# Kernel tuning notes

Measured on AMD Instinct MI355X. Metric: run time of the kernel, lower is better.

## Reference

```python
import jax, jax.numpy as jnp
import numpy as np

B, S, D = 2, 2048, 2048
H, HKV = 16, 4
GROUPS = H // HKV
RQ, RKV = 1024, 512
DH, DR = 192, 64          # q_head_dim, rope dim
DN = DH - DR              # nrope dim = 128
DV = 128                  # v head dim
EPS = 1e-20


def setup_inputs() -> dict:
    key = jax.random.key(0)
    ks = jax.random.split(key, 8)
    inp = {
        "hidden_states": jax.random.normal(ks[0], (B, S, D), jnp.float32),
        # causal mask (0 = masked), as used by masked_fill(mask == 0, -inf)
        "attention_mask": jnp.tril(jnp.ones((S, S), jnp.int32))[None, None],
        "w_qa": jax.random.normal(ks[1], (D, RQ), jnp.float32) * 0.02,
        "b_qa": jnp.zeros((RQ,), jnp.float32),
        "g_q": jnp.ones((RQ,), jnp.float32),
        "w_qb": jax.random.normal(ks[2], (RQ, H * DH), jnp.float32) * 0.02,
        "b_qb": jnp.zeros((H * DH,), jnp.float32),
        "w_kva": jax.random.normal(ks[3], (D, RKV + DR), jnp.float32) * 0.02,
        "b_kva": jnp.zeros((RKV + DR,), jnp.float32),
        "g_kv": jnp.ones((RKV,), jnp.float32),
        "w_kvb": jax.random.normal(ks[4], (RKV, HKV * (DN + DV)), jnp.float32) * 0.02,
        "b_kvb": jnp.zeros((HKV * (DN + DV),), jnp.float32),
        "w_o": jax.random.normal(ks[5], (H * DV, D), jnp.float32) * 0.02,
        "b_o": jnp.zeros((D,), jnp.float32),
    }
    return inp


def _rmsnorm(x, g, eps=EPS):
    var = jnp.mean(x * x, axis=-1, keepdims=True)
    return x * jax.lax.rsqrt(var + eps) * g


def _rope_cos_sin(seq_len, dim, base=10000.0, dtype=jnp.float32):
    inv_freq = 1.0 / (base ** (jnp.arange(0, dim, 2, dtype=jnp.float32) / dim))
    t = jnp.arange(seq_len, dtype=jnp.float32)
    freqs = jnp.outer(t, inv_freq)                    # [S, dim/2]
    emb = jnp.concatenate([freqs, freqs], axis=-1)    # [S, dim]
    return jnp.cos(emb).astype(dtype), jnp.sin(emb).astype(dtype)


def _apply_rope(x, cos, sin):
    # x: [..., S, dr]; rotate_half convention
    d2 = x.shape[-1] // 2
    x1, x2 = x[..., :d2], x[..., d2:]
    rot = jnp.concatenate([-x2, x1], axis=-1)
    return x * cos + rot * sin


def reference(hidden_states, attention_mask, w_qa, b_qa, g_q, w_qb, b_qb,
              w_kva, b_kva, g_kv, w_kvb, b_kvb, w_o, b_o):
    b, s, _ = hidden_states.shape
    # --- Q: LoRA down -> RMSNorm -> LoRA up ---
    q_a = hidden_states @ w_qa + b_qa                         # [B,S,RQ]
    q_b = _rmsnorm(q_a, g_q) @ w_qb + b_qb                    # [B,S,H*DH]
    q_b = q_b.reshape(b, s, H, DH).transpose(0, 2, 1, 3)      # [B,H,S,DH]
    q_nrope, q_rope = q_b[..., :DN], q_b[..., DN:]
    # --- KV: LoRA down, split latent / shared rope key ---
    kv_a = hidden_states @ w_kva + b_kva                      # [B,S,RKV+DR]
    kv_c, k_rope = kv_a[..., :RKV], kv_a[..., RKV:]
    kv_b = _rmsnorm(kv_c, g_kv) @ w_kvb + b_kvb               # [B,S,HKV*(DN+DV)]
    kv_b = kv_b.reshape(b, s, HKV, DN + DV).transpose(0, 2, 1, 3)
    k_nrope, value_states = kv_b[..., :DN], kv_b[..., DN:]    # [B,HKV,S,DN/DV]
    # --- split RoPE ---
    cos, sin = _rope_cos_sin(s, DR, dtype=hidden_states.dtype)
    q_rope = _apply_rope(q_rope, cos, sin)                    # [B,H,S,DR]
    k_rope = _apply_rope(k_rope[:, None], cos, sin)           # [B,1,S,DR]
    # --- assemble heads (rope part first, matching source concat order) ---
    query_states = jnp.concatenate([q_rope, q_nrope], axis=-1)            # [B,H,S,DH]
    key_states = jnp.concatenate(
        [jnp.broadcast_to(k_rope, (b, HKV, s, DR)), k_nrope], axis=-1)    # [B,HKV,S,DH]
    # --- GQA expand kv heads ---
    key_states = jnp.repeat(key_states, GROUPS, axis=1)                   # [B,H,S,DH]
    value_states = jnp.repeat(value_states, GROUPS, axis=1)               # [B,H,S,DV]
    # --- attention ---
    scores = jnp.einsum('bhqd,bhkd->bhqk', query_states, key_states)
    scores = scores / jnp.sqrt(jnp.asarray(DH, scores.dtype))
    scores = jnp.where(attention_mask == 0, jnp.asarray(-1e9, scores.dtype), scores)
    weights = jax.nn.softmax(scores, axis=-1)
    attn_out = jnp.einsum('bhqk,bhkd->bhqd', weights, value_states)       # [B,H,S,DV]
    attn_out = attn_out.transpose(0, 2, 1, 3).reshape(b, s, H * DV)
    return attn_out @ w_o + b_o
```

## Files before the change

### kernel.cpp

```cpp
#include <hip/hip_runtime.h>
#include <hip/hip_bf16.h>
#include <stdint.h>

#define DEV static __device__ __forceinline__

typedef __attribute__((ext_vector_type(8))) short bf16x8;
typedef __attribute__((ext_vector_type(4))) float f32x4;
typedef __attribute__((ext_vector_type(16))) float f32x16;

constexpr int Bc = 2, Sc = 2048, Dc = 2048;
constexpr int Hc = 16, HKVc = 4;
constexpr int RQc = 1024, RKVc = 512;
constexpr int DHc = 192, DRc = 64, DVc = 128;

DEV unsigned short f2bf(float f) {
  union { float f; uint32_t u; } v; v.f = f;
  uint32_t r = v.u + 0x7FFFu + ((v.u >> 16) & 1u);
  return (unsigned short)(r >> 16);
}
DEV float bf2f(unsigned short u) {
  union { uint32_t u; float f; } v; v.u = ((uint32_t)u) << 16;
  return v.f;
}

DEV void gload_lds16(const unsigned short* g, unsigned short* l) {
  __builtin_amdgcn_global_load_lds(
      (const __attribute__((address_space(1))) unsigned int*)g,
      (__attribute__((address_space(3))) unsigned int*)l, 16, 0, 0);
}

__global__ void f2b_kernel(const float* __restrict__ in, unsigned short* __restrict__ out, int n) {
  int stride = gridDim.x * blockDim.x;
  for (int i = blockIdx.x * blockDim.x + threadIdx.x; i * 4 < n; i += stride) {
    float4 v = reinterpret_cast<const float4*>(in)[i];
    union { unsigned short u[4]; uint64_t q; } pk;
    pk.u[0] = f2bf(v.x); pk.u[1] = f2bf(v.y); pk.u[2] = f2bf(v.z); pk.u[3] = f2bf(v.w);
    reinterpret_cast<uint64_t*>(out)[i] = pk.q;
  }
}

__global__ void wtrans_kernel(const float* __restrict__ in, unsigned short* __restrict__ out,
                              int R, int C) {
  __shared__ float tile[32][33];
  const int c0 = blockIdx.x * 32, r0 = blockIdx.y * 32;
  const int tx = threadIdx.x & 31, ty = threadIdx.x >> 5;
#pragma unroll
  for (int i = 0; i < 32; i += 8)
    tile[ty + i][tx] = in[(size_t)(r0 + ty + i) * C + c0 + tx];
  __syncthreads();
#pragma unroll
  for (int i = 0; i < 32; i += 8)
    out[(size_t)(c0 + ty + i) * R + r0 + tx] = f2bf(tile[tx][ty + i]);
}

__global__ void rope_table_kernel(float* __restrict__ cosT, float* __restrict__ sinT) {
  int idx = blockIdx.x * blockDim.x + threadIdx.x;
  if (idx >= Sc * DRc) return;
  int t = idx >> 6;
  int j = idx & 63;
  float inv = exp2f(-13.287712379549449f * (float)(j & 31) * (1.0f / 32.0f));
  float f = (float)t * inv;
  cosT[idx] = cosf(f);
  sinT[idx] = sinf(f);
}

template<int R>
__global__ void rmsnorm_kernel(const float* __restrict__ in, int istride,
                               const float* __restrict__ g, unsigned short* __restrict__ out) {
  int row = blockIdx.x;
  const float* x = in + (size_t)row * istride;
  float ss = 0.f;
  for (int j = threadIdx.x; j < R; j += 256) { float v = x[j]; ss += v * v; }
  for (int off = 32; off; off >>= 1) ss += __shfl_down(ss, off, 64);
  __shared__ float wsum[4];
  if ((threadIdx.x & 63) == 0) wsum[threadIdx.x >> 6] = ss;
  __syncthreads();
  float tot = wsum[0] + wsum[1] + wsum[2] + wsum[3];
  float rs = rsqrtf(tot * (1.0f / R) + 1e-20f);
  for (int j = threadIdx.x; j < R; j += 256)
    out[(size_t)row * R + j] = f2bf(x[j] * rs * g[j]);
}

template<bool OUT_BF16, bool NG>
__global__ __launch_bounds__(256)
void gemm_tn_kernel(const unsigned short* __restrict__ A, const unsigned short* __restrict__ Bt,
                    const float* __restrict__ bias, void* __restrict__ Cout,
                    int M, int N, int K) {
  __shared__ __align__(16) unsigned short As[2][128 * 64];
  __shared__ __align__(16) unsigned short Bs[2][128 * 64];
  const int t = threadIdx.x, lane = t & 63, wave = t >> 6;
  const int wm = wave >> 1, wn = wave & 1;
  const int m0 = blockIdx.x * 128, n0 = blockIdx.y * 128;
  const int fr = lane & 15, fo = (lane >> 4) * 8, rg = lane >> 4;
  const int srow = lane >> 3;
  const int scol = (lane & 7) * 8;

  const unsigned short* Ap[4];
  const unsigned short* Bp[4];
#pragma unroll
  for (int i = 0; i < 4; ++i) {
    const int ar = m0 + wave * 32 + i * 8 + srow;
    Ap[i] = A + (size_t)ar * K + scol;
    int br = n0 + wave * 32 + i * 8 + srow;
    if (NG) br = br < N ? br : N - 1;
    Bp[i] = Bt + (size_t)br * K + scol;
  }

  auto stage = [&](int buf, int k0) {
#pragma unroll
    for (int i = 0; i < 4; ++i) {
      gload_lds16(Ap[i] + k0, &As[buf][(wave * 32 + i * 8) * 64]);
      gload_lds16(Bp[i] + k0, &Bs[buf][(wave * 32 + i * 8) * 64]);
    }
  };

  f32x4 acc[4][4] = {};
  const int nt = K >> 6;

  stage(0, 0);
  for (int tt = 0; tt < nt; ++tt) {
    const int cur = tt & 1;
    if (tt + 1 < nt) {
      stage(cur ^ 1, (tt + 1) * 64);
      asm volatile("s_waitcnt vmcnt(8)" ::: "memory");
    } else {
      asm volatile("s_waitcnt vmcnt(0)" ::: "memory");
    }
    __syncthreads();
#pragma unroll
    for (int kk = 0; kk < 64; kk += 32) {
      bf16x8 af[4], bf[4];
#pragma unroll
      for (int m = 0; m < 4; ++m)
        af[m] = *reinterpret_cast<const bf16x8*>(&As[cur][(wm * 64 + m * 16 + fr) * 64 + kk + fo]);
#pragma unroll
      for (int n = 0; n < 4; ++n)
        bf[n] = *reinterpret_cast<const bf16x8*>(&Bs[cur][(wn * 64 + n * 16 + fr) * 64 + kk + fo]);
      __builtin_amdgcn_s_setprio(1);
#pragma unroll
      for (int m = 0; m < 4; ++m)
#pragma unroll
        for (int n = 0; n < 4; ++n)
          acc[m][n] = __builtin_amdgcn_mfma_f32_16x16x32_bf16(af[m], bf[n], acc[m][n], 0, 0, 0);
      __builtin_amdgcn_s_setprio(0);
    }
    __syncthreads();
  }

#pragma unroll
  for (int m = 0; m < 4; ++m) {
    const int row = m0 + wm * 64 + m * 16 + rg * 4;
#pragma unroll
    for (int n = 0; n < 4; ++n) {
      const int col = n0 + wn * 64 + n * 16 + fr;
      if (NG && col >= N) continue;
      const float bb = bias[col];
#pragma unroll
      for (int r = 0; r < 4; ++r) {
        float v = acc[m][n][r] + bb;
        if (OUT_BF16)
          reinterpret_cast<unsigned short*>(Cout)[(size_t)(row + r) * N + col] = f2bf(v);
        else
          reinterpret_cast<float*>(Cout)[(size_t)(row + r) * N + col] = v;
      }
    }
  }
}

__global__ __launch_bounds__(256)
void gemm_qfuse_kernel(const unsigned short* __restrict__ A, const unsigned short* __restrict__ Bt,
                       const float* __restrict__ bias,
                       const float* __restrict__ cosT, const float* __restrict__ sinT,
                       unsigned short* __restrict__ Qt, int M, int N, int K) {
  const float QS = 0.07216878364870323f * 1.4426950408889634f;
  __shared__ __align__(16) unsigned short As[2][128 * 64];
  __shared__ __align__(16) unsigned short Bs[2][128 * 64];
  const int t = threadIdx.x, lane = t & 63, wave = t >> 6;
  const int wm = wave >> 1, wn = wave & 1;
  const int m0 = blockIdx.x * 128, n0 = blockIdx.y * 128;
  const int fr = lane & 15, fo = (lane >> 4) * 8, rg = lane >> 4;
  const int srow = lane >> 3;
  const int scol = (lane & 7) * 8;

  const unsigned short* Ap[4];
  const unsigned short* Bp[4];
#pragma unroll
  for (int i = 0; i < 4; ++i) {
    Ap[i] = A + (size_t)(m0 + wave * 32 + i * 8 + srow) * K + scol;
    Bp[i] = Bt + (size_t)(n0 + wave * 32 + i * 8 + srow) * K + scol;
  }

  auto stage = [&](int buf, int k0) {
#pragma unroll
    for (int i = 0; i < 4; ++i) {
      gload_lds16(Ap[i] + k0, &As[buf][(wave * 32 + i * 8) * 64]);
      gload_lds16(Bp[i] + k0, &Bs[buf][(wave * 32 + i * 8) * 64]);
    }
  };

  f32x4 acc[4][4] = {};
  const int nt = K >> 6;

  stage(0, 0);
  for (int tt = 0; tt < nt; ++tt) {
    const int cur = tt & 1;
    if (tt + 1 < nt) {
      stage(cur ^ 1, (tt + 1) * 64);
      asm volatile("s_waitcnt vmcnt(8)" ::: "memory");
    } else {
      asm volatile("s_waitcnt vmcnt(0)" ::: "memory");
    }
    __syncthreads();
#pragma unroll
    for (int kk = 0; kk < 64; kk += 32) {
      bf16x8 af[4], bf[4];
#pragma unroll
      for (int m = 0; m < 4; ++m)
        af[m] = *reinterpret_cast<const bf16x8*>(&As[cur][(wm * 64 + m * 16 + fr) * 64 + kk + fo]);
#pragma unroll
      for (int n = 0; n < 4; ++n)
        bf[n] = *reinterpret_cast<const bf16x8*>(&Bs[cur][(wn * 64 + n * 16 + fr) * 64 + kk + fo]);
      __builtin_amdgcn_s_setprio(1);
#pragma unroll
      for (int m = 0; m < 4; ++m)
#pragma unroll
        for (int n = 0; n < 4; ++n)
          acc[m][n] = __builtin_amdgcn_mfma_f32_16x16x32_bf16(af[m], bf[n], acc[m][n], 0, 0, 0);
      __builtin_amdgcn_s_setprio(0);
    }
    __syncthreads();
  }

  const int wbase = n0 + wn * 64;
  const int hq = wbase / 192;
  const int dbase = wbase - hq * 192;
  const bool ropewin = (dbase == 128);

#pragma unroll
  for (int m = 0; m < 4; ++m) {
    const int row0 = m0 + wm * 64 + m * 16 + rg * 4;
#pragma unroll
    for (int n = 0; n < 4; ++n) {
      const int col = wbase + n * 16 + fr;
      const int d = dbase + n * 16 + fr;
      const float bb = bias[col];
#pragma unroll
      for (int r = 0; r < 4; ++r) {
        const int row = row0 + r;
        const int s = row & (Sc - 1);
        const int bq = row >> 11;
        float qv = acc[m][n][r] + bb;
        if (ropewin) {
          const int j = d - 128;
          const int n2 = (n < 2) ? n + 2 : n - 2;
          const float pv = acc[m][n2][r] + bias[wbase + n2 * 16 + fr];
          const float c = cosT[s * 64 + j], sn = sinT[s * 64 + j];
          qv = (n < 2) ? (qv * c - pv * sn) : (qv * c + pv * sn);
        }
        Qt[((size_t)(bq * Hc + hq) * Sc + s) * DHc + d] = f2bf(qv * QS);
      }
    }
  }
}

__global__ void prep_k_kernel(const unsigned short* __restrict__ kvb,
                              const float* __restrict__ ccat,
                              const float* __restrict__ cosT, const float* __restrict__ sinT,
                              unsigned short* __restrict__ K) {
  int bs = blockIdx.x;
  int s = bs & (Sc - 1);
  int b = bs >> 11;
  int d = threadIdx.x;
  if (d >= 192) return;
  unsigned short ropeval = 0;
  if (d >= 128) {
    int j = d - 128;
    float x = ccat[(size_t)bs * 1600 + 1536 + j];
    float other = ccat[(size_t)bs * 1600 + 1536 + (j < 32 ? j + 32 : j - 32)];
    float c = cosT[s * 64 + j], sn = sinT[s * 64 + j];
    float v = (j < 32) ? (x * c - other * sn) : (x * c + other * sn);
    ropeval = f2bf(v);
  }
  const size_t off = (size_t)(s >> 5) * 6144 + (d >> 3) * 256 + (s & 31) * 8 + (d & 7);
  for (int kvh = 0; kvh < HKVc; ++kvh) {
    unsigned short o;
    if (d < 128) o = kvb[(size_t)bs * 1024 + kvh * 256 + d];
    else o = ropeval;
    K[(size_t)(b * HKVc + kvh) * Sc * DHc + off] = o;
  }
}

__global__ void vtrans_kernel(const unsigned short* __restrict__ kvb, unsigned short* __restrict__ Vt) {
  int idx = blockIdx.x;
  int dt = idx & 3;  idx >>= 2;
  int st = idx & 63; idx >>= 6;
  int kvh = idx & 3; idx >>= 2;
  int b = idx;
  __shared__ unsigned short tile[32][33];
  int t = threadIdx.x;
  int c = t & 31, r0 = t >> 5;
#pragma unroll
  for (int i = 0; i < 4; ++i) {
    int r = r0 + i * 8;
    int s = st * 32 + r;
    tile[r][c] = kvb[((size_t)(b * Sc + s)) * 1024 + kvh * 256 + 128 + dt * 32 + c];
  }
  __syncthreads();
#pragma unroll
  for (int i = 0; i < 4; ++i) {
    int r = r0 + i * 8;
    const int dd = dt * 32 + r;
    const int k = st * 32 + c;
    const size_t pos = (size_t)(k >> 5) * 4096 + ((k >> 3) & 3) * 1024 + dd * 8 + (k & 7);
    Vt[(size_t)((b * HKVc + kvh)) * DVc * Sc + pos] = tile[c][r];
  }
}

__global__ __launch_bounds__(128, 3)
void attn_kernel(const unsigned short* __restrict__ Q, const unsigned short* __restrict__ Kt,
                 const unsigned short* __restrict__ Vt, unsigned short* __restrict__ attnOut) {
  __shared__ __align__(16) unsigned short Ks[2][6144];

  const int bid = blockIdx.x;
  const int g = bid & 7;
  const int b = g >> 2, kvh = g & 3;
  const int idx = bid >> 3;
  const int hp = idx & 1;
  const int sub = 63 - (idx >> 1);
  const int w = threadIdx.x >> 6;
  const int h = kvh * 4 + hp * 2 + w;
  const int lane = threadIdx.x & 63;
  const int l31 = lane & 31, hi = lane >> 5;

  const unsigned short* Qh = Q + (size_t)(b * Hc + h) * Sc * DHc;
  const unsigned short* Kg = Kt + (size_t)(b * HKVc + kvh) * Sc * DHc;
  const unsigned short* Vg = Vt + (size_t)(b * HKVc + kvh) * DVc * Sc;

  const int q0 = sub * 32;
  const int q = q0 + l31;
  const int NT = sub + 1;

  auto stage = [&](int t) {
    const unsigned short* src = Kg + (size_t)t * 6144;
    unsigned short* dst = &Ks[t & 1][0];
#pragma unroll
    for (int j = 0; j < 6; ++j) {
      const int jj = w * 6 + j;
      gload_lds16(src + jj * 512 + lane * 8, dst + jj * 512);
    }
  };

  bf16x8 qf[12];
#pragma unroll
  for (int f = 0; f < 12; ++f)
    qf[f] = *reinterpret_cast<const bf16x8*>(Qh + (size_t)q * DHc + f * 16 + hi * 8);

  f32x16 ot[4] = {};
  float m = -INFINITY, lsum = 0.f;

  stage(0);
  asm volatile("s_waitcnt vmcnt(0)" ::: "memory");
  __syncthreads();

  for (int t = 0; t < NT; ++t) {
    const int cur = t & 1;

    bf16x8 vf[8];
#pragma unroll
    for (int dt = 0; dt < 4; ++dt)
#pragma unroll
      for (int k2 = 0; k2 < 2; ++k2)
        vf[dt * 2 + k2] = *reinterpret_cast<const bf16x8*>(
            Vg + (size_t)t * 4096 + (k2 * 2 + hi) * 1024 + (dt * 32 + l31) * 8);
    __builtin_amdgcn_sched_barrier(0);
    if (t + 1 < NT) stage(t + 1);
    __builtin_amdgcn_sched_barrier(0);

    const unsigned short* kb = &Ks[cur][0];
    f32x16 s = {};
    __builtin_amdgcn_s_setprio(1);
#pragma unroll
    for (int f = 0; f < 12; ++f) {
      bf16x8 kf = *reinterpret_cast<const bf16x8*>(kb + (f * 2 + hi) * 256 + l31 * 8);
      s = __builtin_amdgcn_mfma_f32_32x32x16_bf16(kf, qf[f], s, 0, 0, 0);
    }
    __builtin_amdgcn_s_setprio(0);

    float v[16];
    if (t == sub) {
#pragma unroll
      for (int rrr = 0; rrr < 16; ++rrr) {
        const int kl = (rrr & 3) + 8 * (rrr >> 2) + 4 * hi;
        v[rrr] = (kl <= l31) ? s[rrr] : -3.0e38f;
      }
    } else {
#pragma unroll
      for (int rrr = 0; rrr < 16; ++rrr) v[rrr] = s[rrr];
    }

    float pmax = fmaxf(fmaxf(fmaxf(v[0], v[1]), fmaxf(v[2], v[3])),
                       fmaxf(fmaxf(v[4], v[5]), fmaxf(v[6], v[7])));
    float pmax2 = fmaxf(fmaxf(fmaxf(v[8], v[9]), fmaxf(v[10], v[11])),
                        fmaxf(fmaxf(v[12], v[13]), fmaxf(v[14], v[15])));
    pmax = fmaxf(pmax, pmax2);
    pmax = fmaxf(pmax, __shfl_xor(pmax, 32, 64));

    float cf = 1.f;
    if (!__all(pmax - m <= 8.0f)) {
      const float mnew = fmaxf(m, pmax);
      cf = exp2f(m - mnew);
      m = mnew;
#pragma unroll
      for (int dt = 0; dt < 4; ++dt)
#pragma unroll
        for (int rrr = 0; rrr < 16; ++rrr) ot[dt][rrr] *= cf;
    }

    float pp[16];
    float rs = 0.f;
#pragma unroll
    for (int rrr = 0; rrr < 16; ++rrr) { pp[rrr] = exp2f(v[rrr] - m); rs += pp[rrr]; }
    rs += __shfl_xor(rs, 32, 64);
    lsum = lsum * cf + rs;

    uint32_t c[8], x[8];
#pragma unroll
    for (int ii = 0; ii < 8; ++ii) {
      asm("v_cvt_pk_bf16_f32 %0, %1, %2" : "=v"(c[ii]) : "v"(pp[2 * ii]), "v"(pp[2 * ii + 1]));
      x[ii] = (uint32_t)__shfl_xor((int)c[ii], 32, 64);
    }
    union { uint32_t w[4]; bf16x8 v8; } pa0, pa1;
    pa0.w[0] = hi ? x[2] : c[0];
    pa0.w[1] = hi ? x[3] : c[1];
    pa0.w[2] = hi ? c[2] : x[0];
    pa0.w[3] = hi ? c[3] : x[1];
    pa1.w[0] = hi ? x[6] : c[4];
    pa1.w[1] = hi ? x[7] : c[5];
    pa1.w[2] = hi ? c[6] : x[4];
    pa1.w[3] = hi ? c[7] : x[5];

    __builtin_amdgcn_s_setprio(1);
#pragma unroll
    for (int dt = 0; dt < 4; ++dt) {
      ot[dt] = __builtin_amdgcn_mfma_f32_32x32x16_bf16(vf[dt * 2], pa0.v8, ot[dt], 0, 0, 0);
      ot[dt] = __builtin_amdgcn_mfma_f32_32x32x16_bf16(vf[dt * 2 + 1], pa1.v8, ot[dt], 0, 0, 0);
    }
    __builtin_amdgcn_s_setprio(0);

    asm volatile("s_waitcnt vmcnt(0)" ::: "memory");
    __syncthreads();
  }

  const float inv = 1.0f / lsum;
  unsigned short* dst = attnOut + ((size_t)(b * Sc + q)) * (Hc * DVc) + h * DVc;
#pragma unroll
  for (int dt = 0; dt < 4; ++dt)
#pragma unroll
    for (int rq = 0; rq < 4; ++rq) {
      uint32_t lo = (uint32_t)f2bf(ot[dt][rq * 4 + 0] * inv) |
                    ((uint32_t)f2bf(ot[dt][rq * 4 + 1] * inv) << 16);
      uint32_t hi2 = (uint32_t)f2bf(ot[dt][rq * 4 + 2] * inv) |
                     ((uint32_t)f2bf(ot[dt][rq * 4 + 3] * inv) << 16);
      uint2 pk; pk.x = lo; pk.y = hi2;
      *reinterpret_cast<uint2*>(dst + dt * 32 + 8 * rq + 4 * hi) = pk;
    }
}

extern "C" void kernel_launch(void* const* d_in, const int* in_sizes, int n_in,
                              void* d_out, int out_size, void* d_ws, size_t ws_size,
                              hipStream_t stream) {
  (void)in_sizes; (void)n_in; (void)out_size; (void)ws_size;
  const float* hidden = (const float*)d_in[0];
  const float* w_qa  = (const float*)d_in[2];
  const float* b_qa  = (const float*)d_in[3];
  const float* g_q   = (const float*)d_in[4];
  const float* w_qb  = (const float*)d_in[5];
  const float* b_qb  = (const float*)d_in[6];
  const float* w_kva = (const float*)d_in[7];
  const float* b_kva = (const float*)d_in[8];
  const float* g_kv  = (const float*)d_in[9];
  const float* w_kvb = (const float*)d_in[10];
  const float* b_kvb = (const float*)d_in[11];
  const float* w_o   = (const float*)d_in[12];
  const float* b_o   = (const float*)d_in[13];
  float* out = (float*)d_out;

  char* ws = (char*)d_ws;
  size_t off = 0;
  auto alloc = [&](size_t bytes) -> void* {
    void* p = ws + off;
    off += (bytes + 255) & ~(size_t)255;
    return p;
  };
  const int MS = Bc * Sc;
  const int NCAT = RQc + RKVc + DRc;

  unsigned short* Xbf   = (unsigned short*)alloc((size_t)MS * Dc * 2);
  unsigned short* Wcat  = (unsigned short*)alloc((size_t)NCAT * Dc * 2);
  unsigned short* WqbT  = (unsigned short*)alloc((size_t)Hc * DHc * RQc * 2);
  unsigned short* WkvbT = (unsigned short*)alloc((size_t)HKVc * 256 * RKVc * 2);
  unsigned short* WoT   = (unsigned short*)alloc((size_t)Dc * Hc * DVc * 2);
  float* bcat = (float*)alloc((size_t)NCAT * 4);
  float* cosT = (float*)alloc((size_t)Sc * DRc * 4);
  float* sinT = (float*)alloc((size_t)Sc * DRc * 4);
  float* Ccat = (float*)alloc((size_t)MS * NCAT * 4);
  unsigned short* qan  = (unsigned short*)alloc((size_t)MS * RQc * 2);
  unsigned short* kvcn = (unsigned short*)alloc((size_t)MS * RKVc * 2);
  unsigned short* kvb  = (unsigned short*)alloc((size_t)MS * HKVc * 256 * 2);
  unsigned short* Qt   = (unsigned short*)alloc((size_t)Bc * Hc * Sc * DHc * 2);
  unsigned short* Kt   = (unsigned short*)alloc((size_t)Bc * HKVc * Sc * DHc * 2);
  unsigned short* Vt   = (unsigned short*)alloc((size_t)Bc * HKVc * DVc * Sc * 2);
  unsigned short* attnb= (unsigned short*)alloc((size_t)MS * Hc * DVc * 2);

  f2b_kernel<<<dim3(512), dim3(256), 0, stream>>>(hidden, Xbf, MS * Dc);
  wtrans_kernel<<<dim3(RQc / 32, Dc / 32), 256, 0, stream>>>(w_qa, Wcat, Dc, RQc);
  wtrans_kernel<<<dim3((RKVc + DRc) / 32, Dc / 32), 256, 0, stream>>>(w_kva, Wcat + (size_t)RQc * Dc, Dc, RKVc + DRc);
  wtrans_kernel<<<dim3(Hc * DHc / 32, RQc / 32), 256, 0, stream>>>(w_qb, WqbT, RQc, Hc * DHc);
  wtrans_kernel<<<dim3(HKVc * 256 / 32, RKVc / 32), 256, 0, stream>>>(w_kvb, WkvbT, RKVc, HKVc * 256);
  wtrans_kernel<<<dim3(Dc / 32, Hc * DVc / 32), 256, 0, stream>>>(w_o, WoT, Hc * DVc, Dc);
  hipMemcpyAsync(bcat, b_qa, (size_t)RQc * 4, hipMemcpyDeviceToDevice, stream);
  hipMemcpyAsync(bcat + RQc, b_kva, (size_t)(RKVc + DRc) * 4, hipMemcpyDeviceToDevice, stream);
  rope_table_kernel<<<dim3(512), dim3(256), 0, stream>>>(cosT, sinT);

  gemm_tn_kernel<false, true><<<dim3(MS / 128, (NCAT + 127) / 128), 256, 0, stream>>>(Xbf, Wcat, bcat, Ccat, MS, NCAT, Dc);
  rmsnorm_kernel<1024><<<dim3(MS), 256, 0, stream>>>(Ccat, NCAT, g_q, qan);
  rmsnorm_kernel<512><<<dim3(MS), 256, 0, stream>>>(Ccat + RQc, NCAT, g_kv, kvcn);
  gemm_qfuse_kernel<<<dim3(MS / 128, Hc * DHc / 128), 256, 0, stream>>>(qan, WqbT, b_qb, cosT, sinT, Qt, MS, Hc * DHc, RQc);
  gemm_tn_kernel<true, false><<<dim3(MS / 128, HKVc * 256 / 128), 256, 0, stream>>>(kvcn, WkvbT, b_kvb, kvb, MS, HKVc * 256, RKVc);

  prep_k_kernel<<<dim3(MS), 256, 0, stream>>>(kvb, Ccat, cosT, sinT, Kt);
  vtrans_kernel<<<dim3(Bc * HKVc * (Sc / 32) * (DVc / 32)), 256, 0, stream>>>(kvb, Vt);

  attn_kernel<<<dim3(1024), dim3(128), 0, stream>>>(Qt, Kt, Vt, attnb);

  gemm_tn_kernel<false, false><<<dim3(MS / 128, Dc / 128), 256, 0, stream>>>(attnb, WoT, b_o, out, MS, Dc, Hc * DVc);
}
```

Before: 349.8 us.

## Replace double-buffered LDS staging with single-buffer load-then-compute in GEMMs

Both the generic TN GEMM and the fused Q-projection GEMM drop the two-stage LDS ring and prefetch. Each K-tile is now loaded, fully waited on with vmcnt(0), and then computed from a single LDS buffer. This halves shared memory per block, which may allow more resident blocks per CU and lets other waves hide latency. The cost is that global loads no longer overlap MFMA work within a block.

After: 322.3 us. 7.9% less time.

```diff
diff --git a/kernel.cpp b/kernel.cpp
--- a/kernel.cpp
+++ b/kernel.cpp
@@ -86,8 +86,8 @@
 void gemm_tn_kernel(const unsigned short* __restrict__ A, const unsigned short* __restrict__ Bt,
                     const float* __restrict__ bias, void* __restrict__ Cout,
                     int M, int N, int K) {
-  __shared__ __align__(16) unsigned short As[2][128 * 64];
-  __shared__ __align__(16) unsigned short Bs[2][128 * 64];
+  __shared__ __align__(16) unsigned short As[128 * 64];
+  __shared__ __align__(16) unsigned short Bs[128 * 64];
   const int t = threadIdx.x, lane = t & 63, wave = t >> 6;
   const int wm = wave >> 1, wn = wave & 1;
   const int m0 = blockIdx.x * 128, n0 = blockIdx.y * 128;
@@ -106,36 +106,26 @@
     Bp[i] = Bt + (size_t)br * K + scol;
   }
 
-  auto stage = [&](int buf, int k0) {
+  f32x4 acc[4][4] = {};
+
+  for (int k0 = 0; k0 < K; k0 += 64) {
+    if (k0) __syncthreads();
 #pragma unroll
     for (int i = 0; i < 4; ++i) {
-      gload_lds16(Ap[i] + k0, &As[buf][(wave * 32 + i * 8) * 64]);
-      gload_lds16(Bp[i] + k0, &Bs[buf][(wave * 32 + i * 8) * 64]);
-    }
-  };
-
-  f32x4 acc[4][4] = {};
-  const int nt = K >> 6;
-
-  stage(0, 0);
-  for (int tt = 0; tt < nt; ++tt) {
-    const int cur = tt & 1;
-    if (tt + 1 < nt) {
-      stage(cur ^ 1, (tt + 1) * 64);
-      asm volatile("s_waitcnt vmcnt(8)" ::: "memory");
-    } else {
-      asm volatile("s_waitcnt vmcnt(0)" ::: "memory");
-    }
+      gload_lds16(Ap[i] + k0, &As[(wave * 32 + i * 8) * 64]);
+      gload_lds16(Bp[i] + k0, &Bs[(wave * 32 + i * 8) * 64]);
+    }
+    asm volatile("s_waitcnt vmcnt(0)" ::: "memory");
     __syncthreads();
 #pragma unroll
     for (int kk = 0; kk < 64; kk += 32) {
       bf16x8 af[4], bf[4];
 #pragma unroll
       for (int m = 0; m < 4; ++m)
-        af[m] = *reinterpret_cast<const bf16x8*>(&As[cur][(wm * 64 + m * 16 + fr) * 64 + kk + fo]);
+        af[m] = *reinterpret_cast<const bf16x8*>(&As[(wm * 64 + m * 16 + fr) * 64 + kk + fo]);
 #pragma unroll
       for (int n = 0; n < 4; ++n)
-        bf[n] = *reinterpret_cast<const bf16x8*>(&Bs[cur][(wn * 64 + n * 16 + fr) * 64 + kk + fo]);
+        bf[n] = *reinterpret_cast<const bf16x8*>(&Bs[(wn * 64 + n * 16 + fr) * 64 + kk + fo]);
       __builtin_amdgcn_s_setprio(1);
 #pragma unroll
       for (int m = 0; m < 4; ++m)
@@ -144,7 +134,6 @@
           acc[m][n] = __builtin_amdgcn_mfma_f32_16x16x32_bf16(af[m], bf[n], acc[m][n], 0, 0, 0);
       __builtin_amdgcn_s_setprio(0);
     }
-    __syncthreads();
   }
 
 #pragma unroll
@@ -173,8 +162,8 @@
                        const float* __restrict__ cosT, const float* __restrict__ sinT,
                        unsigned short* __restrict__ Qt, int M, int N, int K) {
   const float QS = 0.07216878364870323f * 1.4426950408889634f;
-  __shared__ __align__(16) unsigned short As[2][128 * 64];
-  __shared__ __align__(16) unsigned short Bs[2][128 * 64];
+  __shared__ __align__(16) unsigned short As[128 * 64];
+  __shared__ __align__(16) unsigned short Bs[128 * 64];
   const int t = threadIdx.x, lane = t & 63, wave = t >> 6;
   const int wm = wave >> 1, wn = wave & 1;
   const int m0 = blockIdx.x * 128, n0 = blockIdx.y * 128;
@@ -190,36 +179,26 @@
     Bp[i] = Bt + (size_t)(n0 + wave * 32 + i * 8 + srow) * K + scol;
   }
 
-  auto stage = [&](int buf, int k0) {
+  f32x4 acc[4][4] = {};
+
+  for (int k0 = 0; k0 < K; k0 += 64) {
+    if (k0) __syncthreads();
 #pragma unroll
     for (int i = 0; i < 4; ++i) {
-      gload_lds16(Ap[i] + k0, &As[buf][(wave * 32 + i * 8) * 64]);
-      gload_lds16(Bp[i] + k0, &Bs[buf][(wave * 32 + i * 8) * 64]);
-    }
-  };
-
-  f32x4 acc[4][4] = {};
-  const int nt = K >> 6;
-
-  stage(0, 0);
-  for (int tt = 0; tt < nt; ++tt) {
-    const int cur = tt & 1;
-    if (tt + 1 < nt) {
-      stage(cur ^ 1, (tt + 1) * 64);
-      asm volatile("s_waitcnt vmcnt(8)" ::: "memory");
-    } else {
-      asm volatile("s_waitcnt vmcnt(0)" ::: "memory");
-    }
+      gload_lds16(Ap[i] + k0, &As[(wave * 32 + i * 8) * 64]);
+      gload_lds16(Bp[i] + k0, &Bs[(wave * 32 + i * 8) * 64]);
+    }
+    asm volatile("s_waitcnt vmcnt(0)" ::: "memory");
     __syncthreads();
 #pragma unroll
     for (int kk = 0; kk < 64; kk += 32) {
       bf16x8 af[4], bf[4];
 #pragma unroll
       for (int m = 0; m < 4; ++m)
-        af[m] = *reinterpret_cast<const bf16x8*>(&As[cur][(wm * 64 + m * 16 + fr) * 64 + kk + fo]);
+        af[m] = *reinterpret_cast<const bf16x8*>(&As[(wm * 64 + m * 16 + fr) * 64 + kk + fo]);
 #pragma unroll
       for (int n = 0; n < 4; ++n)
-        bf[n] = *reinterpret_cast<const bf16x8*>(&Bs[cur][(wn * 64 + n * 16 + fr) * 64 + kk + fo]);
+        bf[n] = *reinterpret_cast<const bf16x8*>(&Bs[(wn * 64 + n * 16 + fr) * 64 + kk + fo]);
       __builtin_amdgcn_s_setprio(1);
 #pragma unroll
       for (int m = 0; m < 4; ++m)
@@ -228,7 +207,6 @@
           acc[m][n] = __builtin_amdgcn_mfma_f32_16x16x32_bf16(af[m], bf[n], acc[m][n], 0, 0, 0);
       __builtin_amdgcn_s_setprio(0);
     }
-    __syncthreads();
   }
 
   const int wbase = n0 + wn * 64;
```
